# Optimization experiments

Hardware: AMD Instinct MI355X
Metric: run time of the kernel (lower is better)

## Reference

```python
import jax, jax.numpy as jnp
import numpy as np

RCUT = 6.0
EPS = 1e-6
NUM_BASIS = 8
P = 6  # PolynomialSmooth envelope power
N_NODES = 100000
N_EDGES = 3200000
N_GRAPHS = 16

# 27 periodic image shifts: all integer combos of [-1,0,1]^3
_PERIODIC = jnp.asarray(
    np.stack(np.meshgrid(*([[-1, 0, 1]] * 3), indexing='ij'), -1).reshape(27, 3).astype(np.float32)
)


def _sh_lmax2(u):
    """e3nn spherical harmonics, lmax=2, normalize=True, normalization='component'.
    u: [E,3] unit vectors -> [E,9]."""
    x, y, z = u[..., 0], u[..., 1], u[..., 2]
    s3 = jnp.sqrt(jnp.asarray(3.0, u.dtype))
    s5 = jnp.sqrt(jnp.asarray(5.0, u.dtype))
    s15 = jnp.sqrt(jnp.asarray(15.0, u.dtype))
    return jnp.stack([
        jnp.ones_like(x),                      # l=0
        s3 * x, s3 * y, s3 * z,                # l=1
        s15 * x * z,                           # l=2
        s15 * x * y,
        s5 * (y * y - 0.5 * (x * x + z * z)),
        s15 * y * z,
        0.5 * s15 * (z * z - x * x),
    ], axis=-1)


def _bessel(lengths):
    # lengths: [E,1] -> [E,NUM_BASIS]
    k = jnp.arange(1, NUM_BASIS + 1, dtype=lengths.dtype) * jnp.pi / RCUT
    safe = jnp.clip(lengths, EPS, RCUT)
    return jnp.sin(safe * k) / (2.0 * safe)


def _poly_smooth(lengths):
    # standard polynomial envelope (DimeNet-style), zero at r=rcut
    x = jnp.clip(lengths / RCUT, 0.0, 1.0)
    c1 = (P + 1) * (P + 2) / 2.0
    c2 = float(P * (P + 2))
    c3 = P * (P + 1) / 2.0
    xp = x ** P
    return 1.0 - c1 * xp + c2 * xp * x - c3 * xp * x * x


def setup_inputs() -> dict:
    key = jax.random.key(0)
    k1, k2, k3, k4, k5 = jax.random.split(key, 5)
    pos = jax.random.normal(k1, (N_NODES, 3), dtype=jnp.float32) * 5.0
    cells = jax.random.normal(k2, (N_GRAPHS, 3, 3), dtype=jnp.float32)
    edge_index = jax.random.randint(k3, (2, N_EDGES), 0, N_NODES)
    periodic_index = jax.random.randint(k4, (N_EDGES,), 0, 27)
    batch = jnp.sort(jax.random.randint(k5, (N_NODES,), 0, N_GRAPHS))
    return {"pos": pos, "cells": cells, "edge_index": edge_index,
            "periodic_index": periodic_index, "batch": batch}


def reference(pos, cells, edge_index, periodic_index, batch):
    node_src, node_dst = edge_index[0], edge_index[1]
    vectors = pos[node_dst] - pos[node_src]                     # [E,3]
    shifts = _PERIODIC[periodic_index]                          # [E,3]
    src_cells = cells[batch[node_src]]                          # [E,3,3]
    vectors = vectors - jnp.einsum('eij,ei->ej', src_cells, shifts)
    vectors = -vectors                                          # dst == 'atom'
    lengths = jnp.linalg.norm(vectors, axis=-1, keepdims=True)  # [E,1]
    unit = vectors / jnp.maximum(lengths, EPS)                  # normalize=True
    attr = _sh_lmax2(unit)                                      # [E,9]
    basis = _bessel(lengths)                                    # [E,8]
    cutoff = _poly_smooth(lengths)                              # [E,1]
    basis_weight = basis * cutoff                               # [E,8]
    # pack (length, sh attr, smooth, basis_weight) -> [E,19]
    return jnp.concatenate([lengths, attr, cutoff, basis_weight], axis=-1)
```

## Files before the change

### kernel.cpp

```cpp
#include <hip/hip_runtime.h>

#define BLOCK 256

__global__ __launch_bounds__(BLOCK) void edge_encoding_kernel(
    const float* __restrict__ pos,
    const float* __restrict__ cells,
    const int*  __restrict__ eidx,
    const int*  __restrict__ pidx,
    const int*  __restrict__ batch,
    float* __restrict__ out,
    int E)
{
    __shared__ float s_cells[144];
    __shared__ __align__(16) float s_out[BLOCK * 19];

    const int tid = threadIdx.x;
    if (tid < 144) s_cells[tid] = cells[tid];
    __syncthreads();

    const int base = blockIdx.x * BLOCK;
    const int e = base + tid;

    float row[19];
    if (e < E) {
        const int src = eidx[e];
        const int dst = eidx[E + e];
        const int p   = pidx[e];
        const int g   = batch[src];

        const float sx = pos[3*src+0], sy = pos[3*src+1], sz = pos[3*src+2];
        const float dx = pos[3*dst+0], dy = pos[3*dst+1], dz = pos[3*dst+2];

        const float f0 = (float)(p / 9 - 1);
        const float f1 = (float)((p / 3) % 3 - 1);
        const float f2 = (float)(p % 3 - 1);

        const float* C = s_cells + g * 9;
        const float tx = C[0]*f0 + C[3]*f1 + C[6]*f2;
        const float ty = C[1]*f0 + C[4]*f1 + C[7]*f2;
        const float tz = C[2]*f0 + C[5]*f1 + C[8]*f2;

        const float vx = sx - dx + tx;
        const float vy = sy - dy + ty;
        const float vz = sz - dz + tz;

        const float len  = sqrtf(vx*vx + vy*vy + vz*vz);
        const float invl = 1.0f / fmaxf(len, 1e-6f);
        const float x = vx * invl, y = vy * invl, z = vz * invl;

        const float s3  = 1.7320508075688772f;
        const float s5  = 2.2360679774997896f;
        const float s15 = 3.872983346207417f;

        row[0] = len;
        row[1] = 1.0f;
        row[2] = s3 * x;
        row[3] = s3 * y;
        row[4] = s3 * z;
        row[5] = s15 * x * z;
        row[6] = s15 * x * y;
        row[7] = s5  * (y*y - 0.5f*(x*x + z*z));
        row[8] = s15 * y * z;
        row[9] = 0.5f * s15 * (z*z - x*x);

        const float xc = fminf(len * (1.0f/6.0f), 1.0f);
        const float x3 = xc * xc * xc;
        const float x6 = x3 * x3;
        const float cut = fmaf(x6, fmaf(xc, fmaf(-21.0f, xc, 48.0f), -28.0f), 1.0f);
        row[10] = cut;

        const float safe = fminf(fmaxf(len, 1e-6f), 6.0f);
        const float a = safe * 0.5235987755982988f;
        float sa, ca;
        __sincosf(a, &sa, &ca);
        const float w = cut / (2.0f * safe);
        const float two_ca = 2.0f * ca;
        float s_prev = 0.0f, s_cur = sa;
        row[11] = s_cur * w;
        #pragma unroll
        for (int n = 2; n <= 8; ++n) {
            const float s_next = two_ca * s_cur - s_prev;
            s_prev = s_cur;
            s_cur  = s_next;
            row[10 + n] = s_cur * w;
        }
    } else {
        #pragma unroll
        for (int j = 0; j < 19; ++j) row[j] = 0.0f;
    }

    #pragma unroll
    for (int j = 0; j < 19; ++j) s_out[tid * 19 + j] = row[j];
    __syncthreads();

    const int nvalid  = min(BLOCK, E - base);
    const int nfloats = nvalid * 19;
    float* gout = out + (size_t)base * 19;
    const int n4 = nfloats >> 2;
    const float4* s4 = reinterpret_cast<const float4*>(s_out);
    float4* g4 = reinterpret_cast<float4*>(gout);
    for (int i = tid; i < n4; i += BLOCK) g4[i] = s4[i];
    for (int i = (n4 << 2) + tid; i < nfloats; i += BLOCK) gout[i] = s_out[i];
}

extern "C" void kernel_launch(void* const* d_in, const int* in_sizes, int n_in,
                              void* d_out, int out_size, void* d_ws, size_t ws_size,
                              hipStream_t stream) {
    const float* pos   = (const float*)d_in[0];
    const float* cells = (const float*)d_in[1];
    const int*   eidx  = (const int*)d_in[2];
    const int*   pidx  = (const int*)d_in[3];
    const int*   batch = (const int*)d_in[4];
    float* out = (float*)d_out;

    const int E = in_sizes[3];
    const int grid = (E + BLOCK - 1) / BLOCK;
    edge_encoding_kernel<<<grid, BLOCK, 0, stream>>>(pos, cells, eidx, pidx, batch, out, E);
}
```

Baseline: 316.7 us.

## Process four edges per thread with vector loads and direct nontemporal stores

Each thread now handles four consecutive edges, loading the index arrays as int4 vectors and issuing all gathers before computing. Each thread writes its 76 output floats straight to global memory as 19 float4 nontemporal stores, so the shared-memory staging buffer and its block barrier are gone. The intent is fewer load instructions, more memory-level parallelism and less shared-memory traffic. The cost is higher register pressure and a quarter as many threads. Each thread's stores also span 304 contiguous bytes, so a wavefront's stores are strided rather than fully coalesced.

```diff
diff --git a/kernel.cpp b/kernel.cpp
--- a/kernel.cpp
+++ b/kernel.cpp
@@ -1,6 +1,68 @@
 #include <hip/hip_runtime.h>
 
 #define BLOCK 256
+#define EPT 4
+
+typedef float v4f __attribute__((ext_vector_type(4)));
+typedef int   v4i __attribute__((ext_vector_type(4)));
+
+__device__ __forceinline__ void compute_row(
+    float sx, float sy, float sz, float dx, float dy, float dz,
+    const float* __restrict__ C, int p, float* __restrict__ row)
+{
+    const float f0 = (float)(p / 9 - 1);
+    const float f1 = (float)((p / 3) % 3 - 1);
+    const float f2 = (float)(p % 3 - 1);
+
+    const float tx = C[0]*f0 + C[3]*f1 + C[6]*f2;
+    const float ty = C[1]*f0 + C[4]*f1 + C[7]*f2;
+    const float tz = C[2]*f0 + C[5]*f1 + C[8]*f2;
+
+    const float vx = sx - dx + tx;
+    const float vy = sy - dy + ty;
+    const float vz = sz - dz + tz;
+
+    const float len  = sqrtf(vx*vx + vy*vy + vz*vz);
+    const float invl = 1.0f / fmaxf(len, 1e-6f);
+    const float x = vx * invl, y = vy * invl, z = vz * invl;
+
+    const float s3  = 1.7320508075688772f;
+    const float s5  = 2.2360679774997896f;
+    const float s15 = 3.872983346207417f;
+
+    row[0] = len;
+    row[1] = 1.0f;
+    row[2] = s3 * x;
+    row[3] = s3 * y;
+    row[4] = s3 * z;
+    row[5] = s15 * x * z;
+    row[6] = s15 * x * y;
+    row[7] = s5  * (y*y - 0.5f*(x*x + z*z));
+    row[8] = s15 * y * z;
+    row[9] = 0.5f * s15 * (z*z - x*x);
+
+    const float xc = fminf(len * (1.0f/6.0f), 1.0f);
+    const float x3 = xc * xc * xc;
+    const float x6 = x3 * x3;
+    const float cut = fmaf(x6, fmaf(xc, fmaf(-21.0f, xc, 48.0f), -28.0f), 1.0f);
+    row[10] = cut;
+
+    const float safe = fminf(fmaxf(len, 1e-6f), 6.0f);
+    const float a = safe * 0.5235987755982988f;
+    float sa, ca;
+    __sincosf(a, &sa, &ca);
+    const float w = cut / (2.0f * safe);
+    const float two_ca = 2.0f * ca;
+    float s_prev = 0.0f, s_cur = sa;
+    row[11] = s_cur * w;
+    #pragma unroll
+    for (int n = 2; n <= 8; ++n) {
+        const float s_next = two_ca * s_cur - s_prev;
+        s_prev = s_cur;
+        s_cur  = s_next;
+        row[10 + n] = s_cur * w;
+    }
+}
 
 __global__ __launch_bounds__(BLOCK) void edge_encoding_kernel(
     const float* __restrict__ pos,
@@ -9,98 +71,61 @@
     const int*  __restrict__ pidx,
     const int*  __restrict__ batch,
     float* __restrict__ out,
-    int E)
+    int E, int aligned)
 {
     __shared__ float s_cells[144];
-    __shared__ __align__(16) float s_out[BLOCK * 19];
-
     const int tid = threadIdx.x;
     if (tid < 144) s_cells[tid] = cells[tid];
     __syncthreads();
 
-    const int base = blockIdx.x * BLOCK;
-    const int e = base + tid;
+    const long long e0 = ((long long)blockIdx.x * BLOCK + tid) * EPT;
 
-    float row[19];
-    if (e < E) {
-        const int src = eidx[e];
-        const int dst = eidx[E + e];
-        const int p   = pidx[e];
-        const int g   = batch[src];
+    if (aligned && e0 + EPT <= (long long)E) {
+        const v4i s4i = *reinterpret_cast<const v4i*>(eidx + e0);
+        const v4i d4i = *reinterpret_cast<const v4i*>(eidx + (long long)E + e0);
+        const v4i p4i = *reinterpret_cast<const v4i*>(pidx + e0);
+        const int sidx[EPT] = { s4i.x, s4i.y, s4i.z, s4i.w };
+        const int didx[EPT] = { d4i.x, d4i.y, d4i.z, d4i.w };
+        const int pp[EPT]   = { p4i.x, p4i.y, p4i.z, p4i.w };
 
-        const float sx = pos[3*src+0], sy = pos[3*src+1], sz = pos[3*src+2];
-        const float dx = pos[3*dst+0], dy = pos[3*dst+1], dz = pos[3*dst+2];
+        float S[EPT][3], D[EPT][3];
+        int   G[EPT];
+        #pragma unroll
+        for (int j = 0; j < EPT; ++j) {
+            G[j] = batch[sidx[j]];
+            S[j][0] = pos[3*sidx[j]+0]; S[j][1] = pos[3*sidx[j]+1]; S[j][2] = pos[3*sidx[j]+2];
+            D[j][0] = pos[3*didx[j]+0]; D[j][1] = pos[3*didx[j]+1]; D[j][2] = pos[3*didx[j]+2];
+        }
 
-        const float f0 = (float)(p / 9 - 1);
-        const float f1 = (float)((p / 3) % 3 - 1);
-        const float f2 = (float)(p % 3 - 1);
+        float buf[EPT * 19];
+        #pragma unroll
+        for (int j = 0; j < EPT; ++j) {
+            compute_row(S[j][0], S[j][1], S[j][2], D[j][0], D[j][1], D[j][2],
+                        s_cells + G[j] * 9, pp[j], buf + j * 19);
+        }
 
-        const float* C = s_cells + g * 9;
-        const float tx = C[0]*f0 + C[3]*f1 + C[6]*f2;
-        const float ty = C[1]*f0 + C[4]*f1 + C[7]*f2;
-        const float tz = C[2]*f0 + C[5]*f1 + C[8]*f2;
-
-        const float vx = sx - dx + tx;
-        const float vy = sy - dy + ty;
-        const float vz = sz - dz + tz;
-
-        const float len  = sqrtf(vx*vx + vy*vy + vz*vz);
-        const float invl = 1.0f / fmaxf(len, 1e-6f);
-        const float x = vx * invl, y = vy * invl, z = vz * invl;
-
-        const float s3  = 1.7320508075688772f;
-        const float s5  = 2.2360679774997896f;
-        const float s15 = 3.872983346207417f;
-
-        row[0] = len;
-        row[1] = 1.0f;
-        row[2] = s3 * x;
-        row[3] = s3 * y;
-        row[4] = s3 * z;
-        row[5] = s15 * x * z;
-        row[6] = s15 * x * y;
-        row[7] = s5  * (y*y - 0.5f*(x*x + z*z));
-        row[8] = s15 * y * z;
-        row[9] = 0.5f * s15 * (z*z - x*x);
-
-        const float xc = fminf(len * (1.0f/6.0f), 1.0f);
-        const float x3 = xc * xc * xc;
-        const float x6 = x3 * x3;
-        const float cut = fmaf(x6, fmaf(xc, fmaf(-21.0f, xc, 48.0f), -28.0f), 1.0f);
-        row[10] = cut;
-
-        const float safe = fminf(fmaxf(len, 1e-6f), 6.0f);
-        const float a = safe * 0.5235987755982988f;
-        float sa, ca;
-        __sincosf(a, &sa, &ca);
-        const float w = cut / (2.0f * safe);
-        const float two_ca = 2.0f * ca;
-        float s_prev = 0.0f, s_cur = sa;
-        row[11] = s_cur * w;
+        v4f* o4 = reinterpret_cast<v4f*>(out + e0 * 19);
         #pragma unroll
-        for (int n = 2; n <= 8; ++n) {
-            const float s_next = two_ca * s_cur - s_prev;
-            s_prev = s_cur;
-            s_cur  = s_next;
-            row[10 + n] = s_cur * w;
+        for (int i = 0; i < 19; ++i) {
+            v4f v;
+            v.x = buf[4*i+0]; v.y = buf[4*i+1]; v.z = buf[4*i+2]; v.w = buf[4*i+3];
+            __builtin_nontemporal_store(v, o4 + i);
         }
     } else {
-        #pragma unroll
-        for (int j = 0; j < 19; ++j) row[j] = 0.0f;
+        for (long long e = e0; e < e0 + EPT && e < (long long)E; ++e) {
+            const int src = eidx[e];
+            const int dst = eidx[(long long)E + e];
+            const int p   = pidx[e];
+            const int g   = batch[src];
+            float row[19];
+            compute_row(pos[3*src+0], pos[3*src+1], pos[3*src+2],
+                        pos[3*dst+0], pos[3*dst+1], pos[3*dst+2],
+                        s_cells + g * 9, p, row);
+            float* o = out + e * 19;
+            #pragma unroll
+            for (int j = 0; j < 19; ++j) o[j] = row[j];
+        }
     }
-
-    #pragma unroll
-    for (int j = 0; j < 19; ++j) s_out[tid * 19 + j] = row[j];
-    __syncthreads();
-
-    const int nvalid  = min(BLOCK, E - base);
-    const int nfloats = nvalid * 19;
-    float* gout = out + (size_t)base * 19;
-    const int n4 = nfloats >> 2;
-    const float4* s4 = reinterpret_cast<const float4*>(s_out);
-    float4* g4 = reinterpret_cast<float4*>(gout);
-    for (int i = tid; i < n4; i += BLOCK) g4[i] = s4[i];
-    for (int i = (n4 << 2) + tid; i < nfloats; i += BLOCK) gout[i] = s_out[i];
 }
 
 extern "C" void kernel_launch(void* const* d_in, const int* in_sizes, int n_in,
@@ -114,6 +139,8 @@
     float* out = (float*)d_out;
 
     const int E = in_sizes[3];
-    const int grid = (E + BLOCK - 1) / BLOCK;
-    edge_encoding_kernel<<<grid, BLOCK, 0, stream>>>(pos, cells, eidx, pidx, batch, out, E);
+    const int aligned = (E % 4 == 0) ? 1 : 0;
+    const int per_block = BLOCK * EPT;
+    const int grid = (E + per_block - 1) / per_block;
+    edge_encoding_kernel<<<grid, BLOCK, 0, stream>>>(pos, cells, eidx, pidx, batch, out, E, aligned);
 }
```

After: 869.4 us. 175% more time.
